# Kernel optimization log

Hardware: AMD Instinct MI355X
Metric: run time of the kernel (lower is better)

The kernel has to match this reference:

```python
import jax, jax.numpy as jnp
import numpy as np


def setup_inputs() -> dict:
    key = jax.random.key(0)
    k1, k2 = jax.random.split(key)
    B, S, D, O = 4, 4096, 2048, 2048
    inputs = jax.random.normal(k1, (B, S, D), dtype=jnp.float32)
    # truncated-normal-like init with stddev 1/sqrt(fan_in)
    w = jax.random.normal(k2, (D, O), dtype=jnp.float32) * (1.0 / np.sqrt(D))
    b = jnp.zeros((O,), dtype=jnp.float32)
    return {"inputs": inputs, "w": w, "b": b}


def reference(inputs, w, b):
    # logsumexp-semiring linear layer (basis=None path):
    #   out = log(exp(inputs - max_in) @ exp(w - max_w)) + max_in + max_w + b
    max_inputs = jnp.max(inputs)          # global scalar max for stabilization
    max_w = jnp.max(w)
    exp_inputs = jnp.exp(inputs - max_inputs)   # [B, S, D]
    exp_w = jnp.exp(w - max_w)                  # [D, O]
    out = jnp.log(jnp.dot(exp_inputs, exp_w))   # [B, S, O]
    out = out + (max_inputs + max_w)
    out = out + b                               # broadcast bias over [B, S, O]
    return out
```

## Files before the change

### kernel.cpp

```cpp
#include <hip/hip_runtime.h>

typedef int   i32x4v __attribute__((ext_vector_type(4)));
typedef int   i32x8v __attribute__((ext_vector_type(8)));
typedef float f32x16 __attribute__((ext_vector_type(16)));

#define GLOBAL_AS(p) ((const __attribute__((address_space(1))) void*)(p))
#define LDS_AS(p)    ((__attribute__((address_space(3))) void*)(p))
#define BAR()     __builtin_amdgcn_s_barrier()
#define VMCNT(n)  asm volatile("s_waitcnt vmcnt(" #n ")" ::: "memory")

__device__ inline int fp4_code(float v) {
  return (v > 0.25f) + (v > 0.75f) + (v > 1.25f) + (v > 1.75f) +
         (v > 2.5f) + (v > 3.5f) + (v > 5.0f);
}

__global__ void expcvt_a4_kernel(const float* __restrict__ x,
                                 unsigned char* __restrict__ A4,
                                 unsigned char* __restrict__ SAt,
                                 int M, int K) {
  const int NKB = K >> 5;
  const int t = blockIdx.x * blockDim.x + threadIdx.x;
  const int m = t / NKB, kb = t - m * NKB;
  if (m >= M) return;
  const float4* xs4 = (const float4*)(x + (size_t)m * K + kb * 32);
  float a[32];
  float bm = -3.0e38f;
#pragma unroll
  for (int j = 0; j < 8; ++j) {
    float4 v = xs4[j];
    a[4 * j] = v.x; a[4 * j + 1] = v.y; a[4 * j + 2] = v.z; a[4 * j + 3] = v.w;
    bm = fmaxf(bm, fmaxf(fmaxf(v.x, v.y), fmaxf(v.z, v.w)));
  }
  int e = (int)ceilf(bm * 1.44269504f - 2.58496250f);
  e = min(127, max(-126, e));
  SAt[(size_t)kb * M + ((m >> 7) << 7) + ((m & 31) << 2) + ((m >> 5) & 3)] =
      (unsigned char)(e + 127);
  uint4 u;
  unsigned d[4];
#pragma unroll
  for (int g = 0; g < 4; ++g) {
    unsigned acc = 0;
#pragma unroll
    for (int j = 0; j < 8; ++j) {
      float v = exp2f(a[g * 8 + j] * 1.44269504f - (float)e);
      acc |= (unsigned)fp4_code(v) << (4 * j);
    }
    d[g] = acc;
  }
  u.x = d[0]; u.y = d[1]; u.z = d[2]; u.w = d[3];
  *(uint4*)(A4 + (size_t)m * (K >> 1) + kb * 16) = u;
}

__global__ void expcvt_wt4_kernel(const float* __restrict__ w,
                                  unsigned char* __restrict__ Bt4,
                                  unsigned char* __restrict__ SBt,
                                  int D, int O) {
  __shared__ float tile[32][33];
  int c0 = blockIdx.x * 32;
  int r0 = blockIdx.y * 32;
  int tx = threadIdx.x;
  int ty = threadIdx.y;
#pragma unroll
  for (int j = 0; j < 4; ++j) {
    int r = r0 + ty + j * 8;
    tile[ty + j * 8][tx] = __expf(w[(size_t)r * O + c0 + tx]);
  }
  __syncthreads();
  if (ty == 0) {
    const int n = c0 + tx;
    float bm = 0.0f;
#pragma unroll
    for (int d = 0; d < 32; ++d) bm = fmaxf(bm, tile[d][tx]);
    int e = (int)ceilf(__log2f(bm) - 2.58496250f);
    e = min(127, max(-126, e));
    SBt[(size_t)(r0 >> 5) * O + ((n >> 7) << 7) + ((n & 31) << 2) +
        ((n >> 5) & 3)] = (unsigned char)(e + 127);
    const float inv = exp2f(-(float)e);
    uint4 u;
    unsigned d4[4];
#pragma unroll
    for (int g = 0; g < 4; ++g) {
      unsigned acc = 0;
#pragma unroll
      for (int j = 0; j < 8; ++j)
        acc |= (unsigned)fp4_code(tile[g * 8 + j][tx] * inv) << (4 * j);
      d4[g] = acc;
    }
    u.x = d4[0]; u.y = d4[1]; u.z = d4[2]; u.w = d4[3];
    *(uint4*)(Bt4 + (size_t)n * (D >> 1) + (r0 >> 1)) = u;
  }
}


#define MFMA4(MB, NB, AV, BV, SAv, SBv)                                      \
  acc[MB][NB] = __builtin_amdgcn_mfma_scale_f32_32x32x64_f8f6f4(             \
      AV, BV, acc[MB][NB], 4, 4, 0, SAv, 0, SBv);

__global__ __launch_bounds__(256, 3) void gemm_mx4c_kernel(
    const unsigned char* __restrict__ A4, const unsigned char* __restrict__ Bt4,
    const unsigned char* __restrict__ SAt, const unsigned char* __restrict__ SBt,
    const float* __restrict__ bias, float* __restrict__ out,
    int M, int N, int K) {
  __shared__ char lds[52224];

  const int tid = threadIdx.x;
  const int wid = tid >> 6, lane = tid & 63;
  const int wr = wid >> 1, wc = wid & 1;
  const int l31 = lane & 31, lk = lane >> 5;
  const int NTK = K >> 7;
  const size_t Kb = (size_t)K >> 1;

  const int cpx = gridDim.x >> 3;
  const int v   = (blockIdx.x & 7) * cpx + (blockIdx.x >> 3);
  const int nbn = N >> 7;
  const int bm  = v / nbn, bn = v % nbn;
  const int brow = bm << 7, bcol = bn << 7;

  const int swz = ((l31 & 6) << 3) ^ (l31 & 16);
  const int cR0 = (lk << 5) ^ swz;

  const char* gA[2];
  const char* gB[2];
#pragma unroll
  for (int i = 0; i < 2; ++i) {
    const int o = i * 4096 + tid * 16, row = o >> 6;
    const int sg = (((row & 6) << 3) ^ (row & 16)) >> 4;
    const int gl = ((o >> 4) & 3) ^ sg;
    const int gs = ((gl & 1) << 1) | (gl >> 1);
    gA[i] = (const char*)A4 + (size_t)(brow + row) * Kb + (gs << 4);
    gB[i] = (const char*)Bt4 + (size_t)(bcol + row) * Kb + (gs << 4);
  }
  const char* gS;
  size_t sstep;
  if (wid < 2) {
    gS = (const char*)SAt + ((size_t)(lane >> 5) + 2 * wid) * M + brow + l31 * 4;
    sstep = 4 * (size_t)M;
  } else {
    gS = (const char*)SBt + ((size_t)(lane >> 5) + 2 * (wid - 2)) * N + bcol +
         l31 * 4;
    sstep = 4 * (size_t)N;
  }

  auto STAGE = [&](int t, char* base) {
    const int tt = (t < NTK) ? t : NTK - 1;
    const int koff = tt << 6;
#pragma unroll
    for (int i = 0; i < 2; ++i) {
      __builtin_amdgcn_global_load_lds(GLOBAL_AS(gA[i] + koff),
          LDS_AS(base + i * 4096 + wid * 1024), 16, 0, 0);
      __builtin_amdgcn_global_load_lds(GLOBAL_AS(gB[i] + koff),
          LDS_AS(base + 8192 + i * 4096 + wid * 1024), 16, 0, 0);
    }
    __builtin_amdgcn_global_load_lds(GLOBAL_AS(gS + (size_t)tt * sstep),
        LDS_AS(base + 16384 + wid * 256 + lane * 4), 4, 0, 0);
  };

  f32x16 acc[2][2];
#pragma unroll
  for (int m = 0; m < 2; ++m)
#pragma unroll
    for (int n = 0; n < 2; ++n) acc[m][n] = (f32x16)0.0f;

  char* L0 = lds;
  char* L1 = lds + 17408;
  char* L2 = lds + 34816;

  STAGE(0, L0);
  STAGE(1, L1);
  VMCNT(5);
  BAR();

  const int shA = wr << 4;
  const int shB = wc << 4;

  for (int t = 0; t < NTK; ++t) {
    STAGE(t + 2, L2);

    const char* bA = L0 + wr * 4096;
    const char* bB = L0 + 8192 + wc * 4096;
#pragma unroll
    for (int h = 0; h < 2; ++h) {
      const int ch = cR0 ^ (h << 4);
      i32x8v a8[2], b8[2];
#pragma unroll
      for (int mb = 0; mb < 2; ++mb) {
        i32x4v f = *(const i32x4v*)(bA + (mb * 32 + l31) * 64 + ch);
        a8[mb] = __builtin_shufflevector(f, f, 0, 1, 2, 3, -1, -1, -1, -1);
      }
#pragma unroll
      for (int nb = 0; nb < 2; ++nb) {
        i32x4v f = *(const i32x4v*)(bB + (nb * 32 + l31) * 64 + ch);
        b8[nb] = __builtin_shufflevector(f, f, 0, 1, 2, 3, -1, -1, -1, -1);
      }
      const int kb2 = 2 * h + lk;
      const int saw = *(const int*)(L0 + 16384 + kb2 * 128 + l31 * 4);
      const int sbw = *(const int*)(L0 + 16896 + kb2 * 128 + l31 * 4);
      const int sA0 = (saw >> shA) & 0xFF, sA1 = (saw >> (shA + 8)) & 0xFF;
      const int sB0 = (sbw >> shB) & 0xFF, sB1 = (sbw >> (shB + 8)) & 0xFF;
      MFMA4(0, 0, a8[0], b8[0], sA0, sB0)
      MFMA4(1, 0, a8[1], b8[0], sA1, sB0)
      MFMA4(0, 1, a8[0], b8[1], sA0, sB1)
      MFMA4(1, 1, a8[1], b8[1], sA1, sB1)
    }

    VMCNT(5);
    BAR();
    char* sw = L0; L0 = L1; L1 = L2; L2 = sw;
  }

  const int col0 = bcol + wc * 64 + l31;
  const int row0 = brow + wr * 64 + lk * 4;
  const float bv0 = bias[col0], bv1 = bias[col0 + 32];
#pragma unroll
  for (int mb = 0; mb < 2; ++mb) {
#pragma unroll
    for (int rg = 0; rg < 16; ++rg) {
      const int row = row0 + mb * 32 + (rg & 3) + 8 * (rg >> 2);
      const size_t ro = (size_t)row * N + col0;
      __builtin_nontemporal_store(__logf(acc[mb][0][rg]) + bv0, &out[ro]);
      __builtin_nontemporal_store(__logf(acc[mb][1][rg]) + bv1, &out[ro + 32]);
    }
  }
}

extern "C" void kernel_launch(void* const* d_in, const int* in_sizes, int n_in,
                              void* d_out, int out_size, void* d_ws, size_t ws_size,
                              hipStream_t stream) {
  const float* inputs = (const float*)d_in[0];
  const float* w      = (const float*)d_in[1];
  const float* bias   = (const float*)d_in[2];
  float* out = (float*)d_out;

  const int O = in_sizes[2];
  const int D = in_sizes[1] / O;
  const size_t MD = (size_t)in_sizes[0];
  const int M = (int)(MD / (size_t)D);

  unsigned char* ws  = (unsigned char*)d_ws;
  unsigned char* A4  = ws;
  unsigned char* Bt4 = ws + MD / 2;
  unsigned char* SAt = Bt4 + (size_t)O * D / 2;
  unsigned char* SBt = SAt + MD / 32;

  const int nthr = (int)((MD / 32 + 255) / 256);
  expcvt_a4_kernel<<<nthr, 256, 0, stream>>>(inputs, A4, SAt, M, D);

  dim3 tg(O / 32, D / 32);
  expcvt_wt4_kernel<<<tg, dim3(32, 8), 0, stream>>>(w, Bt4, SBt, D, O);

  dim3 grid((M / 128) * (O / 128));
  gemm_mx4c_kernel<<<grid, 256, 0, stream>>>(A4, Bt4, SAt, SBt, bias, out,
                                             M, O, D);
}
```

Before: 90.47 us.

## Switch GEMM to double-buffered LDS pipeline to fit four blocks per CU

Replaces the three-stage LDS ring with a two-stage ping-pong buffer unrolled by two, shrinking shared memory per block. It raises the launch bound from three to four blocks per CU so more waves can hide latency. In exchange, prefetch depth drops to one tile and an extra barrier per tile is added before overwriting the buffer being read.

```diff
diff --git a/kernel.cpp b/kernel.cpp
--- a/kernel.cpp
+++ b/kernel.cpp
@@ -96,12 +96,12 @@
   acc[MB][NB] = __builtin_amdgcn_mfma_scale_f32_32x32x64_f8f6f4(             \
       AV, BV, acc[MB][NB], 4, 4, 0, SAv, 0, SBv);
 
-__global__ __launch_bounds__(256, 3) void gemm_mx4c_kernel(
+__global__ __launch_bounds__(256, 4) void gemm_mx4d_kernel(
     const unsigned char* __restrict__ A4, const unsigned char* __restrict__ Bt4,
     const unsigned char* __restrict__ SAt, const unsigned char* __restrict__ SBt,
     const float* __restrict__ bias, float* __restrict__ out,
     int M, int N, int K) {
-  __shared__ char lds[52224];
+  __shared__ char lds[34816];
 
   const int tid = threadIdx.x;
   const int wid = tid >> 6, lane = tid & 63;
@@ -161,23 +161,12 @@
 #pragma unroll
     for (int n = 0; n < 2; ++n) acc[m][n] = (f32x16)0.0f;
 
-  char* L0 = lds;
-  char* L1 = lds + 17408;
-  char* L2 = lds + 34816;
-
-  STAGE(0, L0);
-  STAGE(1, L1);
-  VMCNT(5);
-  BAR();
-
   const int shA = wr << 4;
   const int shB = wc << 4;
 
-  for (int t = 0; t < NTK; ++t) {
-    STAGE(t + 2, L2);
-
-    const char* bA = L0 + wr * 4096;
-    const char* bB = L0 + 8192 + wc * 4096;
+  auto COMPUTE = [&](const char* base) {
+    const char* bA = base + wr * 4096;
+    const char* bB = base + 8192 + wc * 4096;
 #pragma unroll
     for (int h = 0; h < 2; ++h) {
       const int ch = cR0 ^ (h << 4);
@@ -193,8 +182,8 @@
         b8[nb] = __builtin_shufflevector(f, f, 0, 1, 2, 3, -1, -1, -1, -1);
       }
       const int kb2 = 2 * h + lk;
-      const int saw = *(const int*)(L0 + 16384 + kb2 * 128 + l31 * 4);
-      const int sbw = *(const int*)(L0 + 16896 + kb2 * 128 + l31 * 4);
+      const int saw = *(const int*)(base + 16384 + kb2 * 128 + l31 * 4);
+      const int sbw = *(const int*)(base + 16896 + kb2 * 128 + l31 * 4);
       const int sA0 = (saw >> shA) & 0xFF, sA1 = (saw >> (shA + 8)) & 0xFF;
       const int sB0 = (sbw >> shB) & 0xFF, sB1 = (sbw >> (shB + 8)) & 0xFF;
       MFMA4(0, 0, a8[0], b8[0], sA0, sB0)
@@ -202,11 +191,27 @@
       MFMA4(0, 1, a8[0], b8[1], sA0, sB1)
       MFMA4(1, 1, a8[1], b8[1], sA1, sB1)
     }
-
+  };
+
+  char* const L0 = lds;
+  char* const L1 = lds + 17408;
+
+  STAGE(0, L0);
+
+  for (int j = 0; j < (NTK >> 1); ++j) {
+    STAGE(2 * j + 1, L1);
     VMCNT(5);
     BAR();
-    char* sw = L0; L0 = L1; L1 = L2; L2 = sw;
-  }
+    COMPUTE(L0);
+    BAR();
+    STAGE(2 * j + 2, L0);
+    VMCNT(5);
+    BAR();
+    COMPUTE(L1);
+    BAR();
+  }
+
+  VMCNT(0);
 
   const int col0 = bcol + wc * 64 + l31;
   const int row0 = brow + wr * 64 + lk * 4;
@@ -249,6 +254,6 @@
   expcvt_wt4_kernel<<<tg, dim3(32, 8), 0, stream>>>(w, Bt4, SBt, D, O);
 
   dim3 grid((M / 128) * (O / 128));
-  gemm_mx4c_kernel<<<grid, 256, 0, stream>>>(A4, Bt4, SAt, SBt, bias, out,
+  gemm_mx4d_kernel<<<grid, 256, 0, stream>>>(A4, Bt4, SAt, SBt, bias, out,
                                              M, O, D);
 }
```

New measurement: 88.79 us. About the same (-1.9%).
